# Optimization experiments

Measured on AMD Instinct MI355X. Metric: run time of the kernel, lower is better.

The kernel has to match this reference:

```python
import jax, jax.numpy as jnp
import numpy as np

V, E, NNZ = 50000, 25000, 200000
F_IN, HID, D = 128, 256, 4
H1, C = 16, 40  # h = [256, 16, 40] per the code's width schedule for l=2


def setup_inputs() -> dict:
    key = jax.random.key(0)
    ks = jax.random.split(key, 16)
    inp = {
        'x': jax.random.normal(ks[0], (V, F_IN), jnp.float32),
        'eattr': jax.random.normal(ks[1], (E, F_IN), jnp.float32),  # init_hedge='rand'
        'node_idx': jax.random.randint(ks[2], (NNZ,), 0, V),
        'edge_idx': jax.random.randint(ks[3], (NNZ,), 0, E),
        # lin: F_IN -> D*HID (shared for nodes and hyperedge attrs)
        'Wlin': jax.random.normal(ks[4], (F_IN, D * HID), jnp.float32) / np.sqrt(F_IN),
        'blin': jnp.zeros((D * HID,), jnp.float32),
        # diag sheaf builder: per-incidence, per-head restriction-map scalar
        'w1': jax.random.normal(ks[5], (HID, D), jnp.float32) / np.sqrt(HID),
        'w2': jax.random.normal(ks[6], (HID, D), jnp.float32) / np.sqrt(HID),
        'bs': jnp.zeros((D,), jnp.float32),
        # hypergraph conv layers
        'W0': jax.random.normal(ks[7], (HID, H1), jnp.float32) / np.sqrt(HID),
        'b0': jnp.zeros((H1,), jnp.float32),
        'W1': jax.random.normal(ks[8], (H1, C), jnp.float32) / np.sqrt(H1),
        'b1': jnp.zeros((C,), jnp.float32),
        # lin2: h[-1]*d -> num_classes, no bias
        'W2': jax.random.normal(ks[9], (D * C, C), jnp.float32) / np.sqrt(D * C),
    }
    return inp


def reference(x, eattr, node_idx, edge_idx, Wlin, blin, w1, w2, bs, W0, b0, W1, b1, W2):
    # lift node / hyperedge features into d stalks: [V, d, HID], [E, d, HID]
    Hn = (x @ Wlin + blin).reshape(V, D, HID)
    He = (eattr @ Wlin + blin).reshape(E, D, HID)

    # diagonal sheaf restriction maps, one scalar per (incidence, head)
    hv = Hn[node_idx]                      # [NNZ, D, HID] gather
    he = He[edge_idx]                      # [NNZ, D, HID] gather
    s = jnp.tanh(jnp.einsum('ndh,hd->nd', hv, w1)
                 + jnp.einsum('ndh,hd->nd', he, w2) + bs)   # [NNZ, D]

    # degree normalization (degree_norm): D^{-1}, inf -> 0
    deg_e = jax.ops.segment_sum(jnp.ones((NNZ,), jnp.float32), edge_idx, num_segments=E)
    inv_e = jnp.where(deg_e > 0, 1.0 / deg_e, 0.0)
    deg_v = jax.ops.segment_sum(jnp.ones((NNZ,), jnp.float32), node_idx, num_segments=V)
    inv_v = jnp.where(deg_v > 0, 1.0 / deg_v, 0.0)

    def apply_L(Hf):  # sheaf Laplacian L = I - D^{-1} F^T B F : [V, D, c] -> [V, D, c]
        m = jax.ops.segment_sum(s[:, :, None] * Hf[node_idx], edge_idx, num_segments=E)
        m = m * inv_e[:, None, None]       # hyperedge aggregation [E, D, c]
        a = jax.ops.segment_sum(s[:, :, None] * m[edge_idx], node_idx, num_segments=V)
        a = a * inv_v[:, None, None]       # back-scatter to nodes [V, D, c]
        return Hf - a

    H = jax.nn.relu(apply_L(Hn) @ W0 + b0)   # [V, D, 16]
    H = jax.nn.relu(apply_L(H) @ W1 + b1)    # [V, D, 40]
    return H.reshape(V, D * C) @ W2          # [V, 40]
```

## Files before the change

kernel.cpp:

```cpp
#include <hip/hip_runtime.h>
#include <hip/hip_fp16.h>
#include <stdint.h>

#define V_N 50000
#define E_N 25000
#define NNZ_N 200000
#define CHUNK 2048

__global__ __launch_bounds__(256) void k_zero(int* __restrict__ p, int n) {
  int i = blockIdx.x * 256 + threadIdx.x;
  if (i < n) p[i] = 0;
}

__global__ __launch_bounds__(64) void k_fuse(
    const float* __restrict__ Wlin, const float* __restrict__ blin,
    const float* __restrict__ w1, const float* __restrict__ w2,
    const float* __restrict__ bs, const float* __restrict__ W0,
    const float* __restrict__ b0,
    float* __restrict__ Wf0, float* __restrict__ u1, float* __restrict__ u2,
    float* __restrict__ cb, float* __restrict__ bf0, float* __restrict__ sbias)
{
  __shared__ float row[1024];
  __shared__ float W0s[4096];
  int f = blockIdx.x;
  for (int t = threadIdx.x; t < 1024; t += 64) row[t] = Wlin[f * 1024 + t];
  for (int t = threadIdx.x; t < 4096; t += 64) W0s[t] = W0[t];
  __syncthreads();
  int j = threadIdx.x;
  int d = j >> 4, jj = j & 15;
  float acc = 0.f;
  for (int h = 0; h < 256; ++h) acc += row[d * 256 + h] * W0s[h * 16 + jj];
  Wf0[f * 64 + j] = acc;
  if (j < 4) {
    float a1 = 0.f, a2 = 0.f;
    for (int h = 0; h < 256; ++h) {
      a1 += row[j * 256 + h] * w1[h * 4 + j];
      a2 += row[j * 256 + h] * w2[h * 4 + j];
    }
    u1[f * 4 + j] = a1;
    u2[f * 4 + j] = a2;
  }
  if (f == 0) {
    float ab = 0.f;
    for (int h = 0; h < 256; ++h) ab += blin[d * 256 + h] * W0s[h * 16 + jj];
    cb[j] = ab;
    bf0[j] = b0[jj];
    if (j < 4) {
      float sb = bs[j];
      for (int h = 0; h < 256; ++h) sb += blin[j * 256 + h] * (w1[h * 4 + j] + w2[h * 4 + j]);
      sbias[j] = sb;
    }
  }
}

__global__ __launch_bounds__(256) void k_degrees(
    const int* __restrict__ node_idx, const int* __restrict__ edge_idx,
    int* __restrict__ degE, int* __restrict__ degV)
{
  int i = blockIdx.x * 256 + threadIdx.x;
  if (i < NNZ_N) {
    atomicAdd(&degE[edge_idx[i]], 1);
    atomicAdd(&degV[node_idx[i]], 1);
  }
}

__global__ __launch_bounds__(256) void k_scanA(
    const int* __restrict__ degE, const int* __restrict__ degV,
    int* __restrict__ offE, int* __restrict__ offV,
    int* __restrict__ bsumE, int* __restrict__ bsumV, int nchunkE)
{
  bool isE = (int)blockIdx.x < nchunkE;
  const int* deg = isE ? degE : degV;
  int* off = isE ? offE : offV;
  int* bsum = isE ? bsumE : bsumV;
  int n = isE ? E_N : V_N;
  int chunk = isE ? blockIdx.x : (blockIdx.x - nchunkE);
  int base = chunk * CHUNK;
  int tid = threadIdx.x;
  int vals[8];
  int tsum = 0;
  for (int it = 0; it < 8; ++it) {
    int idx = base + tid * 8 + it;
    int v = (idx < n) ? deg[idx] : 0;
    vals[it] = tsum;
    tsum += v;
  }
  __shared__ int sA[256], sB[256];
  sA[tid] = tsum;
  __syncthreads();
  int* src = sA; int* dst = sB;
  for (int sh = 1; sh < 256; sh <<= 1) {
    dst[tid] = src[tid] + (tid >= sh ? src[tid - sh] : 0);
    __syncthreads();
    int* t = src; src = dst; dst = t;
  }
  int excl = src[tid] - tsum;
  for (int it = 0; it < 8; ++it) {
    int idx = base + tid * 8 + it;
    if (idx < n) off[idx] = excl + vals[it];
  }
  if (tid == 255) bsum[chunk] = src[255];
}

__global__ __launch_bounds__(64) void k_scanB(
    int* __restrict__ bsumE, int* __restrict__ bsumV, int nchunkE, int nchunkV)
{
  int* b = (blockIdx.x == 0) ? bsumE : bsumV;
  int n = (blockIdx.x == 0) ? nchunkE : nchunkV;
  int tid = threadIdx.x;
  int v = (tid < n) ? b[tid] : 0;
  int s = v;
  for (int sh = 1; sh < 64; sh <<= 1) {
    int o = __shfl_up(s, sh);
    if (tid >= sh) s += o;
  }
  if (tid < n) b[tid] = s - v;
}

__global__ __launch_bounds__(256) void k_scanC_inv(
    int* __restrict__ offE, int* __restrict__ offV,
    const int* __restrict__ bsumE, const int* __restrict__ bsumV,
    const int* __restrict__ degE, const int* __restrict__ degV,
    float* __restrict__ invE, float* __restrict__ invV, int nchunkE)
{
  bool isE = (int)blockIdx.x < nchunkE;
  int* off = isE ? offE : offV;
  const int* bsum = isE ? bsumE : bsumV;
  const int* deg = isE ? degE : degV;
  float* inv = isE ? invE : invV;
  int n = isE ? E_N : V_N;
  int chunk = isE ? blockIdx.x : (blockIdx.x - nchunkE);
  int base = chunk * CHUNK;
  int add = bsum[chunk];
  for (int it = 0; it < 8; ++it) {
    int idx = base + threadIdx.x * 8 + it;
    if (idx < n) {
      off[idx] += add;
      int dg = deg[idx];
      inv[idx] = dg > 0 ? 1.0f / (float)dg : 0.0f;
    }
  }
}

__global__ __launch_bounds__(256) void k_gemm_node(
    const float* __restrict__ x, const float* __restrict__ Wf0,
    const float* __restrict__ u1, const float* __restrict__ cb,
    __half* __restrict__ G0h, float* __restrict__ svx)
{
  __shared__ float Xt[64 * 132];
  __shared__ float us[512];
  int tid = threadIdx.x;
  int row0 = blockIdx.x * 64;
  #pragma unroll
  for (int it = 0; it < 8; ++it) {
    int fi = it * 1024 + tid * 4;
    int r = fi >> 7, c = fi & 127;
    float4 val = make_float4(0.f, 0.f, 0.f, 0.f);
    int gr = row0 + r;
    if (gr < V_N) val = *(const float4*)(x + (size_t)gr * 128 + c);
    *(float4*)&Xt[r * 132 + c] = val;
  }
  for (int k2 = tid; k2 < 512; k2 += 256) us[k2] = u1[k2];
  int ty = tid >> 4, tx = tid & 15;
  float4 cbr = *(const float4*)(cb + tx * 4);
  __syncthreads();

  float acc[4][4];
  #pragma unroll
  for (int i = 0; i < 4; ++i) {
    acc[i][0] = cbr.x; acc[i][1] = cbr.y; acc[i][2] = cbr.z; acc[i][3] = cbr.w;
  }
  #pragma unroll 2
  for (int k0 = 0; k0 < 128; k0 += 4) {
    float A_[4][4], W_[4][4];
    #pragma unroll
    for (int kk = 0; kk < 4; ++kk)
      *(float4*)&W_[kk][0] = *(const float4*)(Wf0 + (size_t)(k0 + kk) * 64 + tx * 4);
    #pragma unroll
    for (int i = 0; i < 4; ++i)
      *(float4*)&A_[i][0] = *(const float4*)&Xt[(ty * 4 + i) * 132 + k0];
    #pragma unroll
    for (int i = 0; i < 4; ++i)
      #pragma unroll
      for (int kk = 0; kk < 4; ++kk)
        #pragma unroll
        for (int j = 0; j < 4; ++j)
          acc[i][j] += A_[i][kk] * W_[kk][j];
  }
  #pragma unroll
  for (int i = 0; i < 4; ++i) {
    int gr = row0 + ty * 4 + i;
    if (gr < V_N) {
      __half2* dst = (__half2*)(G0h + (size_t)gr * 64 + tx * 4);
      dst[0] = __floats2half2_rn(acc[i][0], acc[i][1]);
      dst[1] = __floats2half2_rn(acc[i][2], acc[i][3]);
    }
  }
  int rs = tid >> 2, dS = tid & 3;
  float a2 = 0.f;
  for (int k = 0; k < 128; ++k)
    a2 += Xt[rs * 132 + k] * us[k * 4 + dS];
  int gr = row0 + rs;
  if (gr < V_N) svx[gr * 4 + dS] = a2;
}

__global__ __launch_bounds__(256) void k_gemm_edge(
    const float* __restrict__ eattr, const float* __restrict__ u2,
    float* __restrict__ sex)
{
  __shared__ float Xt[64 * 132];
  __shared__ float us[512];
  int tid = threadIdx.x;
  int row0 = blockIdx.x * 64;
  #pragma unroll
  for (int it = 0; it < 8; ++it) {
    int fi = it * 1024 + tid * 4;
    int r = fi >> 7, c = fi & 127;
    float4 val = make_float4(0.f, 0.f, 0.f, 0.f);
    int gr = row0 + r;
    if (gr < E_N) val = *(const float4*)(eattr + (size_t)gr * 128 + c);
    *(float4*)&Xt[r * 132 + c] = val;
  }
  for (int k2 = tid; k2 < 512; k2 += 256) us[k2] = u2[k2];
  __syncthreads();
  int rs = tid >> 2, dS = tid & 3;
  float a2 = 0.f;
  for (int k = 0; k < 128; ++k)
    a2 += Xt[rs * 132 + k] * us[k * 4 + dS];
  int gr = row0 + rs;
  if (gr < E_N) sex[gr * 4 + dS] = a2;
}

__global__ __launch_bounds__(256) void k_fill_s(
    const int* __restrict__ node_idx, const int* __restrict__ edge_idx,
    const int* __restrict__ offE, const int* __restrict__ offV,
    int* __restrict__ curE, int* __restrict__ curV,
    int* __restrict__ csrEv, int* __restrict__ csrVe,
    float* __restrict__ sE4, float* __restrict__ sV4,
    const float* __restrict__ svx, const float* __restrict__ sex,
    const float* __restrict__ sbias,
    const float* __restrict__ invE, const float* __restrict__ invV)
{
  int i = blockIdx.x * 256 + threadIdx.x;
  if (i >= NNZ_N) return;
  int v = node_idx[i], e = edge_idx[i];
  float4 a = *(const float4*)(svx + (size_t)v * 4);
  float4 b = *(const float4*)(sex + (size_t)e * 4);
  float4 sb = *(const float4*)(sbias);
  float4 r;
  r.x = tanhf(a.x + b.x + sb.x);
  r.y = tanhf(a.y + b.y + sb.y);
  r.z = tanhf(a.z + b.z + sb.z);
  r.w = tanhf(a.w + b.w + sb.w);
  float ie = invE[e], iv = invV[v];
  int pe = atomicAdd(&curE[e], 1);
  int slotE = offE[e] + pe;
  csrEv[slotE] = v;
  float4 re = make_float4(r.x * ie, r.y * ie, r.z * ie, r.w * ie);
  *(float4*)(sE4 + (size_t)slotE * 4) = re;
  int pv = atomicAdd(&curV[v], 1);
  int slotV = offV[v] + pv;
  csrVe[slotV] = e;
  float4 rv = make_float4(r.x * iv, r.y * iv, r.z * iv, r.w * iv);
  *(float4*)(sV4 + (size_t)slotV * 4) = rv;
}

__global__ __launch_bounds__(256) void k_eagg(
    const __half* __restrict__ Hin, const int* __restrict__ csrEv,
    const float* __restrict__ sE4,
    const int* __restrict__ offE, const int* __restrict__ degE,
    __half* __restrict__ m)
{
  int wave = threadIdx.x >> 6, lane = threadIdx.x & 63;
  int e = blockIdx.x * 4 + wave;
  if (e >= E_N) return;
  int o0 = offE[e], dg = degE[e];
  int hw = lane >> 3, L8 = lane & 7;
  int d = L8 >> 1;
  float4 a0 = make_float4(0.f, 0.f, 0.f, 0.f);
  float4 a1 = make_float4(0.f, 0.f, 0.f, 0.f);
  for (int base = 0; base < dg; base += 8) {
    int vv = 0;
    if (lane < 8 && base + lane < dg) vv = csrEv[o0 + base + lane];
    float ss = 0.f;
    if (lane < 32 && base * 4 + lane < dg * 4) ss = sE4[(size_t)o0 * 4 + base * 4 + lane];
    int tloc = base + hw;
    int v = __shfl(vv, hw);
    float sv = __shfl(ss, hw * 4 + d);
    if (tloc < dg) {
      uint4 raw = *(const uint4*)(Hin + (size_t)v * 64 + L8 * 8);
      float2 f0 = __half22float2(*reinterpret_cast<__half2*>(&raw.x));
      float2 f1 = __half22float2(*reinterpret_cast<__half2*>(&raw.y));
      float2 f2 = __half22float2(*reinterpret_cast<__half2*>(&raw.z));
      float2 f3 = __half22float2(*reinterpret_cast<__half2*>(&raw.w));
      a0.x += sv * f0.x; a0.y += sv * f0.y; a0.z += sv * f1.x; a0.w += sv * f1.y;
      a1.x += sv * f2.x; a1.y += sv * f2.y; a1.z += sv * f3.x; a1.w += sv * f3.y;
    }
  }
  #pragma unroll
  for (int off = 8; off <= 32; off <<= 1) {
    a0.x += __shfl_xor(a0.x, off); a0.y += __shfl_xor(a0.y, off);
    a0.z += __shfl_xor(a0.z, off); a0.w += __shfl_xor(a0.w, off);
    a1.x += __shfl_xor(a1.x, off); a1.y += __shfl_xor(a1.y, off);
    a1.z += __shfl_xor(a1.z, off); a1.w += __shfl_xor(a1.w, off);
  }
  if (hw == 0) {
    __half2 o0h = __floats2half2_rn(a0.x, a0.y);
    __half2 o1h = __floats2half2_rn(a0.z, a0.w);
    __half2 o2h = __floats2half2_rn(a1.x, a1.y);
    __half2 o3h = __floats2half2_rn(a1.z, a1.w);
    uint4 o;
    o.x = *(unsigned int*)&o0h; o.y = *(unsigned int*)&o1h;
    o.z = *(unsigned int*)&o2h; o.w = *(unsigned int*)&o3h;
    *(uint4*)(m + (size_t)e * 64 + L8 * 8) = o;
  }
}

__global__ __launch_bounds__(256) void k_nagg(
    const __half* __restrict__ base_, const __half* __restrict__ m,
    const int* __restrict__ csrVe, const float* __restrict__ sV4,
    const int* __restrict__ offV, const int* __restrict__ degV,
    const float* __restrict__ bf0, int doRelu,
    __half* __restrict__ outH, float* __restrict__ outF)
{
  int half = threadIdx.x >> 5;
  int v = blockIdx.x * 8 + half;
  if (v >= V_N) return;
  int lane = threadIdx.x & 63;
  int ll = lane & 31;
  int s0 = lane & 32;
  int o0 = offV[v], dg = degV[v];
  int hw = ll >> 3, L8 = ll & 7;
  int d = L8 >> 1;
  float4 a0 = make_float4(0.f, 0.f, 0.f, 0.f);
  float4 a1 = make_float4(0.f, 0.f, 0.f, 0.f);
  for (int base = 0; base < dg; base += 4) {
    int ee = 0;
    if (ll < 4 && base + ll < dg) ee = csrVe[o0 + base + ll];
    float ss = 0.f;
    if (ll < 16 && base * 4 + ll < dg * 4) ss = sV4[(size_t)o0 * 4 + base * 4 + ll];
    int tloc = base + hw;
    int e = __shfl(ee, s0 + hw);
    float sv = __shfl(ss, s0 + hw * 4 + d);
    if (tloc < dg) {
      uint4 raw = *(const uint4*)(m + (size_t)e * 64 + L8 * 8);
      float2 f0 = __half22float2(*reinterpret_cast<__half2*>(&raw.x));
      float2 f1 = __half22float2(*reinterpret_cast<__half2*>(&raw.y));
      float2 f2 = __half22float2(*reinterpret_cast<__half2*>(&raw.z));
      float2 f3 = __half22float2(*reinterpret_cast<__half2*>(&raw.w));
      a0.x += sv * f0.x; a0.y += sv * f0.y; a0.z += sv * f1.x; a0.w += sv * f1.y;
      a1.x += sv * f2.x; a1.y += sv * f2.y; a1.z += sv * f3.x; a1.w += sv * f3.y;
    }
  }
  #pragma unroll
  for (int off = 8; off <= 16; off <<= 1) {
    a0.x += __shfl_xor(a0.x, off); a0.y += __shfl_xor(a0.y, off);
    a0.z += __shfl_xor(a0.z, off); a0.w += __shfl_xor(a0.w, off);
    a1.x += __shfl_xor(a1.x, off); a1.y += __shfl_xor(a1.y, off);
    a1.z += __shfl_xor(a1.z, off); a1.w += __shfl_xor(a1.w, off);
  }
  if (hw == 0) {
    uint4 braw = *(const uint4*)(base_ + (size_t)v * 64 + L8 * 8);
    float2 b0f = __half22float2(*reinterpret_cast<__half2*>(&braw.x));
    float2 b1f = __half22float2(*reinterpret_cast<__half2*>(&braw.y));
    float2 b2f = __half22float2(*reinterpret_cast<__half2*>(&braw.z));
    float2 b3f = __half22float2(*reinterpret_cast<__half2*>(&braw.w));
    float r0 = b0f.x - a0.x, r1 = b0f.y - a0.y, r2 = b1f.x - a0.z, r3 = b1f.y - a0.w;
    float r4 = b2f.x - a1.x, r5 = b2f.y - a1.y, r6 = b3f.x - a1.z, r7 = b3f.y - a1.w;
    if (doRelu) {
      float4 bfa = *(const float4*)(bf0 + L8 * 8);
      float4 bfb = *(const float4*)(bf0 + L8 * 8 + 4);
      r0 = fmaxf(r0 + bfa.x, 0.f); r1 = fmaxf(r1 + bfa.y, 0.f);
      r2 = fmaxf(r2 + bfa.z, 0.f); r3 = fmaxf(r3 + bfa.w, 0.f);
      r4 = fmaxf(r4 + bfb.x, 0.f); r5 = fmaxf(r5 + bfb.y, 0.f);
      r6 = fmaxf(r6 + bfb.z, 0.f); r7 = fmaxf(r7 + bfb.w, 0.f);
      __half2 o0h = __floats2half2_rn(r0, r1);
      __half2 o1h = __floats2half2_rn(r2, r3);
      __half2 o2h = __floats2half2_rn(r4, r5);
      __half2 o3h = __floats2half2_rn(r6, r7);
      uint4 o;
      o.x = *(unsigned int*)&o0h; o.y = *(unsigned int*)&o1h;
      o.z = *(unsigned int*)&o2h; o.w = *(unsigned int*)&o3h;
      *(uint4*)(outH + (size_t)v * 64 + L8 * 8) = o;
    } else {
      *(float4*)(outF + (size_t)v * 64 + L8 * 8) = make_float4(r0, r1, r2, r3);
      *(float4*)(outF + (size_t)v * 64 + L8 * 8 + 4) = make_float4(r4, r5, r6, r7);
    }
  }
}

__global__ __launch_bounds__(256) void k_final(
    const float* __restrict__ A, const float* __restrict__ W1, const float* __restrict__ b1,
    const float* __restrict__ W2, float* __restrict__ out)
{
  __shared__ float W2s[160 * 40];
  __shared__ float t[32 * 164];
  __shared__ float W1s[640];
  __shared__ float b1s[40];
  int tid = threadIdx.x;
  int v0 = blockIdx.x * 32;

  for (int k = tid; k < 1600; k += 256) ((float4*)W2s)[k] = ((const float4*)W2)[k];
  for (int k = tid; k < 640; k += 256) W1s[k] = W1[k];
  if (tid < 40) b1s[tid] = b1[tid];
  __syncthreads();

  if (tid < 160) {
    int rg = tid / 20, cg = tid % 20;
    int r0 = rg * 4;
    int j0 = cg * 8;
    int d = cg / 5;
    int jloc = j0 - d * 40;
    float a[4][16];
    #pragma unroll
    for (int i = 0; i < 4; ++i) {
      int gr = v0 + r0 + i;
      #pragma unroll
      for (int c4 = 0; c4 < 4; ++c4) {
        float4 val = make_float4(0.f, 0.f, 0.f, 0.f);
        if (gr < V_N) val = *(const float4*)(A + (size_t)gr * 64 + d * 16 + c4 * 4);
        *(float4*)&a[i][c4 * 4] = val;
      }
    }
    float acc1[4][8];
    #pragma unroll
    for (int i = 0; i < 4; ++i)
      #pragma unroll
      for (int jj = 0; jj < 8; ++jj) acc1[i][jj] = b1s[jloc + jj];
    #pragma unroll
    for (int c = 0; c < 16; ++c) {
      float w[8];
      *(float4*)&w[0] = *(const float4*)&W1s[c * 40 + jloc];
      *(float4*)&w[4] = *(const float4*)&W1s[c * 40 + jloc + 4];
      #pragma unroll
      for (int i = 0; i < 4; ++i)
        #pragma unroll
        for (int jj = 0; jj < 8; ++jj)
          acc1[i][jj] += a[i][c] * w[jj];
    }
    #pragma unroll
    for (int i = 0; i < 4; ++i) {
      float4 lo = make_float4(fmaxf(acc1[i][0], 0.f), fmaxf(acc1[i][1], 0.f),
                              fmaxf(acc1[i][2], 0.f), fmaxf(acc1[i][3], 0.f));
      float4 hi = make_float4(fmaxf(acc1[i][4], 0.f), fmaxf(acc1[i][5], 0.f),
                              fmaxf(acc1[i][6], 0.f), fmaxf(acc1[i][7], 0.f));
      *(float4*)&t[(r0 + i) * 164 + j0] = lo;
      *(float4*)&t[(r0 + i) * 164 + j0 + 4] = hi;
    }
  }
  __syncthreads();

  if (tid < 160) {
    int rg2 = tid / 10, cg2 = tid % 10;
    float acc2[2][4] = {{0.f, 0.f, 0.f, 0.f}, {0.f, 0.f, 0.f, 0.f}};
    for (int k0 = 0; k0 < 160; k0 += 4) {
      float a0[4], a1[4], w[4][4];
      *(float4*)a0 = *(const float4*)&t[(rg2 * 2 + 0) * 164 + k0];
      *(float4*)a1 = *(const float4*)&t[(rg2 * 2 + 1) * 164 + k0];
      #pragma unroll
      for (int kk = 0; kk < 4; ++kk)
        *(float4*)&w[kk][0] = *(const float4*)&W2s[(k0 + kk) * 40 + cg2 * 4];
      #pragma unroll
      for (int kk = 0; kk < 4; ++kk)
        #pragma unroll
        for (int j = 0; j < 4; ++j) {
          acc2[0][j] += a0[kk] * w[kk][j];
          acc2[1][j] += a1[kk] * w[kk][j];
        }
    }
    #pragma unroll
    for (int i = 0; i < 2; ++i) {
      int gr = v0 + rg2 * 2 + i;
      if (gr < V_N)
        *(float4*)(out + (size_t)gr * 40 + cg2 * 4) =
            make_float4(acc2[i][0], acc2[i][1], acc2[i][2], acc2[i][3]);
    }
  }
}

extern "C" void kernel_launch(void* const* d_in, const int* in_sizes, int n_in,
                              void* d_out, int out_size, void* d_ws, size_t ws_size,
                              hipStream_t stream) {
  (void)in_sizes; (void)n_in; (void)out_size; (void)ws_size;
  const float* x = (const float*)d_in[0];
  const float* eattr = (const float*)d_in[1];
  const int* node_idx = (const int*)d_in[2];
  const int* edge_idx = (const int*)d_in[3];
  const float* Wlin = (const float*)d_in[4];
  const float* blin = (const float*)d_in[5];
  const float* w1 = (const float*)d_in[6];
  const float* w2 = (const float*)d_in[7];
  const float* bs = (const float*)d_in[8];
  const float* W0 = (const float*)d_in[9];
  const float* b0 = (const float*)d_in[10];
  const float* W1 = (const float*)d_in[11];
  const float* b1 = (const float*)d_in[12];
  const float* W2 = (const float*)d_in[13];
  float* out = (float*)d_out;

  char* p = (char*)d_ws;
  auto alloc = [&](size_t bytes) { char* q = p; p += (bytes + 255) & ~(size_t)255; return q; };
  float*  Wf0   = (float*)alloc(8192 * 4);
  float*  u1    = (float*)alloc(512 * 4);
  float*  u2    = (float*)alloc(512 * 4);
  float*  cbv   = (float*)alloc(64 * 4);
  float*  bf0   = (float*)alloc(64 * 4);
  float*  sbias = (float*)alloc(4 * 4);
  __half* G0h   = (__half*)alloc((size_t)V_N * 64 * 2);
  __half* Hbh   = (__half*)alloc((size_t)V_N * 64 * 2);
  __half* mbh   = (__half*)alloc((size_t)E_N * 64 * 2);
  float*  Af    = (float*)alloc((size_t)V_N * 64 * 4);
  float*  svx   = (float*)alloc((size_t)V_N * 4 * 4);
  float*  sex   = (float*)alloc((size_t)E_N * 4 * 4);
  float*  sE4   = (float*)alloc((size_t)NNZ_N * 4 * 4);
  float*  sV4   = (float*)alloc((size_t)NNZ_N * 4 * 4);
  float*  invE  = (float*)alloc(E_N * 4);
  float*  invV  = (float*)alloc(V_N * 4);
  int* zeroRegion = (int*)alloc((size_t)(2 * E_N + 2 * V_N) * 4);
  int* degE = zeroRegion;
  int* degV = degE + E_N;
  int* curE = degV + V_N;
  int* curV = curE + E_N;
  int* offE  = (int*)alloc(E_N * 4);
  int* offV  = (int*)alloc(V_N * 4);
  int* csrEv = (int*)alloc((size_t)NNZ_N * 4);
  int* csrVe = (int*)alloc((size_t)NNZ_N * 4);
  int* bsumE = (int*)alloc(64 * 4);
  int* bsumV = (int*)alloc(64 * 4);

  int nZero = 2 * E_N + 2 * V_N;
  int nchunkE = (E_N + CHUNK - 1) / CHUNK;
  int nchunkV = (V_N + CHUNK - 1) / CHUNK;
  int nbNode = (V_N + 63) / 64;
  int nbEdge = (E_N + 63) / 64;

  hipLaunchKernelGGL(k_zero, dim3((nZero + 255) / 256), dim3(256), 0, stream, zeroRegion, nZero);
  hipLaunchKernelGGL(k_fuse, dim3(128), dim3(64), 0, stream,
                     Wlin, blin, w1, w2, bs, W0, b0, Wf0, u1, u2, cbv, bf0, sbias);
  hipLaunchKernelGGL(k_degrees, dim3((NNZ_N + 255) / 256), dim3(256), 0, stream,
                     node_idx, edge_idx, degE, degV);
  hipLaunchKernelGGL(k_scanA, dim3(nchunkE + nchunkV), dim3(256), 0, stream,
                     degE, degV, offE, offV, bsumE, bsumV, nchunkE);
  hipLaunchKernelGGL(k_scanB, dim3(2), dim3(64), 0, stream, bsumE, bsumV, nchunkE, nchunkV);
  hipLaunchKernelGGL(k_scanC_inv, dim3(nchunkE + nchunkV), dim3(256), 0, stream,
                     offE, offV, bsumE, bsumV, degE, degV, invE, invV, nchunkE);
  hipLaunchKernelGGL(k_gemm_node, dim3(nbNode), dim3(256), 0, stream,
                     x, Wf0, u1, cbv, G0h, svx);
  hipLaunchKernelGGL(k_gemm_edge, dim3(nbEdge), dim3(256), 0, stream,
                     eattr, u2, sex);
  hipLaunchKernelGGL(k_fill_s, dim3((NNZ_N + 255) / 256), dim3(256), 0, stream,
                     node_idx, edge_idx, offE, offV, curE, curV, csrEv, csrVe,
                     sE4, sV4, svx, sex, sbias, invE, invV);
  hipLaunchKernelGGL(k_eagg, dim3((E_N + 3) / 4), dim3(256), 0, stream,
                     G0h, csrEv, sE4, offE, degE, mbh);
  hipLaunchKernelGGL(k_nagg, dim3((V_N + 7) / 8), dim3(256), 0, stream,
                     G0h, mbh, csrVe, sV4, offV, degV, bf0, 1, Hbh, (float*)nullptr);
  hipLaunchKernelGGL(k_eagg, dim3((E_N + 3) / 4), dim3(256), 0, stream,
                     Hbh, csrEv, sE4, offE, degE, mbh);
  hipLaunchKernelGGL(k_nagg, dim3((V_N + 7) / 8), dim3(256), 0, stream,
                     Hbh, mbh, csrVe, sV4, offV, degV, bf0, 0, (__half*)nullptr, Af);
  hipLaunchKernelGGL(k_final, dim3((V_N + 31) / 32), dim3(256), 0, stream, Af, W1, b1, W2, out);
}
```

Baseline: 284.1 us.

## Merge CSR build and aggregation kernels into one cooperative persistent kernel

Replaces the zero, degree, three scan, fill, and four aggregation launches with a single cooperative kernel of 768 blocks that uses grid-wide syncs between phases. The goal is to remove per-launch overhead and the idle gaps between many small dependent kernels. In exchange, every phase now runs on a fixed persistent grid with grid-stride loops, and each grid.sync adds a barrier cost. Occupancy is capped by the launch_bounds(256,3) hint, which can limit latency hiding in the gather-heavy aggregation phases.

New measurement: 1.047 ms. 268% more time.

```diff
diff --git a/kernel.cpp b/kernel.cpp
--- a/kernel.cpp
+++ b/kernel.cpp
@@ -1,16 +1,14 @@
 #include <hip/hip_runtime.h>
 #include <hip/hip_fp16.h>
+#include <hip/hip_cooperative_groups.h>
 #include <stdint.h>
+
+namespace cg = cooperative_groups;
 
 #define V_N 50000
 #define E_N 25000
 #define NNZ_N 200000
 #define CHUNK 2048
-
-__global__ __launch_bounds__(256) void k_zero(int* __restrict__ p, int n) {
-  int i = blockIdx.x * 256 + threadIdx.x;
-  if (i < n) p[i] = 0;
-}
 
 __global__ __launch_bounds__(64) void k_fuse(
     const float* __restrict__ Wlin, const float* __restrict__ blin,
@@ -53,95 +51,6 @@
   }
 }
 
-__global__ __launch_bounds__(256) void k_degrees(
-    const int* __restrict__ node_idx, const int* __restrict__ edge_idx,
-    int* __restrict__ degE, int* __restrict__ degV)
-{
-  int i = blockIdx.x * 256 + threadIdx.x;
-  if (i < NNZ_N) {
-    atomicAdd(&degE[edge_idx[i]], 1);
-    atomicAdd(&degV[node_idx[i]], 1);
-  }
-}
-
-__global__ __launch_bounds__(256) void k_scanA(
-    const int* __restrict__ degE, const int* __restrict__ degV,
-    int* __restrict__ offE, int* __restrict__ offV,
-    int* __restrict__ bsumE, int* __restrict__ bsumV, int nchunkE)
-{
-  bool isE = (int)blockIdx.x < nchunkE;
-  const int* deg = isE ? degE : degV;
-  int* off = isE ? offE : offV;
-  int* bsum = isE ? bsumE : bsumV;
-  int n = isE ? E_N : V_N;
-  int chunk = isE ? blockIdx.x : (blockIdx.x - nchunkE);
-  int base = chunk * CHUNK;
-  int tid = threadIdx.x;
-  int vals[8];
-  int tsum = 0;
-  for (int it = 0; it < 8; ++it) {
-    int idx = base + tid * 8 + it;
-    int v = (idx < n) ? deg[idx] : 0;
-    vals[it] = tsum;
-    tsum += v;
-  }
-  __shared__ int sA[256], sB[256];
-  sA[tid] = tsum;
-  __syncthreads();
-  int* src = sA; int* dst = sB;
-  for (int sh = 1; sh < 256; sh <<= 1) {
-    dst[tid] = src[tid] + (tid >= sh ? src[tid - sh] : 0);
-    __syncthreads();
-    int* t = src; src = dst; dst = t;
-  }
-  int excl = src[tid] - tsum;
-  for (int it = 0; it < 8; ++it) {
-    int idx = base + tid * 8 + it;
-    if (idx < n) off[idx] = excl + vals[it];
-  }
-  if (tid == 255) bsum[chunk] = src[255];
-}
-
-__global__ __launch_bounds__(64) void k_scanB(
-    int* __restrict__ bsumE, int* __restrict__ bsumV, int nchunkE, int nchunkV)
-{
-  int* b = (blockIdx.x == 0) ? bsumE : bsumV;
-  int n = (blockIdx.x == 0) ? nchunkE : nchunkV;
-  int tid = threadIdx.x;
-  int v = (tid < n) ? b[tid] : 0;
-  int s = v;
-  for (int sh = 1; sh < 64; sh <<= 1) {
-    int o = __shfl_up(s, sh);
-    if (tid >= sh) s += o;
-  }
-  if (tid < n) b[tid] = s - v;
-}
-
-__global__ __launch_bounds__(256) void k_scanC_inv(
-    int* __restrict__ offE, int* __restrict__ offV,
-    const int* __restrict__ bsumE, const int* __restrict__ bsumV,
-    const int* __restrict__ degE, const int* __restrict__ degV,
-    float* __restrict__ invE, float* __restrict__ invV, int nchunkE)
-{
-  bool isE = (int)blockIdx.x < nchunkE;
-  int* off = isE ? offE : offV;
-  const int* bsum = isE ? bsumE : bsumV;
-  const int* deg = isE ? degE : degV;
-  float* inv = isE ? invE : invV;
-  int n = isE ? E_N : V_N;
-  int chunk = isE ? blockIdx.x : (blockIdx.x - nchunkE);
-  int base = chunk * CHUNK;
-  int add = bsum[chunk];
-  for (int it = 0; it < 8; ++it) {
-    int idx = base + threadIdx.x * 8 + it;
-    if (idx < n) {
-      off[idx] += add;
-      int dg = deg[idx];
-      inv[idx] = dg > 0 ? 1.0f / (float)dg : 0.0f;
-    }
-  }
-}
-
 __global__ __launch_bounds__(256) void k_gemm_node(
     const float* __restrict__ x, const float* __restrict__ Wf0,
     const float* __restrict__ u1, const float* __restrict__ cb,
@@ -231,49 +140,11 @@
   if (gr < E_N) sex[gr * 4 + dS] = a2;
 }
 
-__global__ __launch_bounds__(256) void k_fill_s(
-    const int* __restrict__ node_idx, const int* __restrict__ edge_idx,
-    const int* __restrict__ offE, const int* __restrict__ offV,
-    int* __restrict__ curE, int* __restrict__ curV,
-    int* __restrict__ csrEv, int* __restrict__ csrVe,
-    float* __restrict__ sE4, float* __restrict__ sV4,
-    const float* __restrict__ svx, const float* __restrict__ sex,
-    const float* __restrict__ sbias,
-    const float* __restrict__ invE, const float* __restrict__ invV)
-{
-  int i = blockIdx.x * 256 + threadIdx.x;
-  if (i >= NNZ_N) return;
-  int v = node_idx[i], e = edge_idx[i];
-  float4 a = *(const float4*)(svx + (size_t)v * 4);
-  float4 b = *(const float4*)(sex + (size_t)e * 4);
-  float4 sb = *(const float4*)(sbias);
-  float4 r;
-  r.x = tanhf(a.x + b.x + sb.x);
-  r.y = tanhf(a.y + b.y + sb.y);
-  r.z = tanhf(a.z + b.z + sb.z);
-  r.w = tanhf(a.w + b.w + sb.w);
-  float ie = invE[e], iv = invV[v];
-  int pe = atomicAdd(&curE[e], 1);
-  int slotE = offE[e] + pe;
-  csrEv[slotE] = v;
-  float4 re = make_float4(r.x * ie, r.y * ie, r.z * ie, r.w * ie);
-  *(float4*)(sE4 + (size_t)slotE * 4) = re;
-  int pv = atomicAdd(&curV[v], 1);
-  int slotV = offV[v] + pv;
-  csrVe[slotV] = e;
-  float4 rv = make_float4(r.x * iv, r.y * iv, r.z * iv, r.w * iv);
-  *(float4*)(sV4 + (size_t)slotV * 4) = rv;
-}
-
-__global__ __launch_bounds__(256) void k_eagg(
-    const __half* __restrict__ Hin, const int* __restrict__ csrEv,
-    const float* __restrict__ sE4,
-    const int* __restrict__ offE, const int* __restrict__ degE,
-    __half* __restrict__ m)
-{
-  int wave = threadIdx.x >> 6, lane = threadIdx.x & 63;
-  int e = blockIdx.x * 4 + wave;
-  if (e >= E_N) return;
+__device__ __forceinline__ void eagg_seg(
+    int e, const __half* __restrict__ Hin, const int* __restrict__ csrEv,
+    const float* __restrict__ sE4, const int* __restrict__ offE,
+    const int* __restrict__ degE, __half* __restrict__ m, int lane)
+{
   int o0 = offE[e], dg = degE[e];
   int hw = lane >> 3, L8 = lane & 7;
   int d = L8 >> 1;
@@ -316,17 +187,13 @@
   }
 }
 
-__global__ __launch_bounds__(256) void k_nagg(
-    const __half* __restrict__ base_, const __half* __restrict__ m,
+__device__ __forceinline__ void nagg_seg(
+    int v, const __half* __restrict__ base_, const __half* __restrict__ m,
     const int* __restrict__ csrVe, const float* __restrict__ sV4,
     const int* __restrict__ offV, const int* __restrict__ degV,
-    const float* __restrict__ bf0, int doRelu,
-    __half* __restrict__ outH, float* __restrict__ outF)
-{
-  int half = threadIdx.x >> 5;
-  int v = blockIdx.x * 8 + half;
-  if (v >= V_N) return;
-  int lane = threadIdx.x & 63;
+    const float* __restrict__ bf0, bool doRelu,
+    __half* __restrict__ outH, float* __restrict__ outF, int lane)
+{
   int ll = lane & 31;
   int s0 = lane & 32;
   int o0 = offV[v], dg = degV[v];
@@ -389,6 +256,153 @@
   }
 }
 
+__global__ __launch_bounds__(256, 3) void k_mega(
+    const int* __restrict__ node_idx, const int* __restrict__ edge_idx,
+    const float* __restrict__ svx, const float* __restrict__ sex,
+    const float* __restrict__ sbias, const float* __restrict__ bf0,
+    int* __restrict__ zeroReg,
+    int* __restrict__ offE, int* __restrict__ offV,
+    int* __restrict__ bsumE, int* __restrict__ bsumV,
+    float* __restrict__ invE, float* __restrict__ invV,
+    int* __restrict__ csrEv, int* __restrict__ csrVe,
+    float* __restrict__ sE4, float* __restrict__ sV4,
+    const __half* __restrict__ G0h, __half* __restrict__ Hbh,
+    __half* __restrict__ mbh, float* __restrict__ Af)
+{
+  cg::grid_group grid = cg::this_grid();
+  int tid = threadIdx.x;
+  const int NB = gridDim.x;
+  const int NT = NB * 256;
+  int gid = blockIdx.x * 256 + tid;
+
+  int* degE = zeroReg;
+  int* degV = degE + E_N;
+  int* curE = degV + V_N;
+  int* curV = curE + E_N;
+
+  __shared__ int sA[256], sB[256];
+
+  for (int i = gid; i < 2 * E_N + 2 * V_N; i += NT) zeroReg[i] = 0;
+  grid.sync();
+
+  for (int i = gid; i < NNZ_N; i += NT) {
+    atomicAdd(&degE[edge_idx[i]], 1);
+    atomicAdd(&degV[node_idx[i]], 1);
+  }
+  grid.sync();
+
+  const int nchE = (E_N + CHUNK - 1) / CHUNK;
+  const int nchV = (V_N + CHUNK - 1) / CHUNK;
+  for (int blk = blockIdx.x; blk < nchE + nchV; blk += NB) {
+    bool isE = blk < nchE;
+    const int* deg = isE ? degE : degV;
+    int* off = isE ? offE : offV;
+    int* bsum = isE ? bsumE : bsumV;
+    int n = isE ? E_N : V_N;
+    int chunk = isE ? blk : blk - nchE;
+    int base = chunk * CHUNK;
+    int vals[8];
+    int tsum = 0;
+    for (int it = 0; it < 8; ++it) {
+      int idx = base + tid * 8 + it;
+      int v = (idx < n) ? deg[idx] : 0;
+      vals[it] = tsum;
+      tsum += v;
+    }
+    __syncthreads();
+    sA[tid] = tsum;
+    __syncthreads();
+    int* src = sA; int* dst = sB;
+    for (int sh = 1; sh < 256; sh <<= 1) {
+      dst[tid] = src[tid] + (tid >= sh ? src[tid - sh] : 0);
+      __syncthreads();
+      int* t = src; src = dst; dst = t;
+    }
+    int excl = src[tid] - tsum;
+    for (int it = 0; it < 8; ++it) {
+      int idx = base + tid * 8 + it;
+      if (idx < n) off[idx] = excl + vals[it];
+    }
+    if (tid == 255) bsum[chunk] = src[255];
+  }
+  grid.sync();
+
+  if (blockIdx.x < 2 && tid < 64) {
+    int* b = (blockIdx.x == 0) ? bsumE : bsumV;
+    int n = (blockIdx.x == 0) ? nchE : nchV;
+    int v = (tid < n) ? b[tid] : 0;
+    int s = v;
+    for (int sh = 1; sh < 64; sh <<= 1) {
+      int o = __shfl_up(s, sh);
+      if (tid >= sh) s += o;
+    }
+    if (tid < n) b[tid] = s - v;
+  }
+  grid.sync();
+
+  for (int blk = blockIdx.x; blk < nchE + nchV; blk += NB) {
+    bool isE = blk < nchE;
+    int* off = isE ? offE : offV;
+    const int* bsum = isE ? bsumE : bsumV;
+    const int* deg = isE ? degE : degV;
+    float* inv = isE ? invE : invV;
+    int n = isE ? E_N : V_N;
+    int chunk = isE ? blk : blk - nchE;
+    int base = chunk * CHUNK;
+    int add = bsum[chunk];
+    for (int it = 0; it < 8; ++it) {
+      int idx = base + tid * 8 + it;
+      if (idx < n) {
+        off[idx] += add;
+        int dg = deg[idx];
+        inv[idx] = dg > 0 ? 1.0f / (float)dg : 0.0f;
+      }
+    }
+  }
+  grid.sync();
+
+  for (int i = gid; i < NNZ_N; i += NT) {
+    int v = node_idx[i], e = edge_idx[i];
+    float4 a = *(const float4*)(svx + (size_t)v * 4);
+    float4 b = *(const float4*)(sex + (size_t)e * 4);
+    float4 sb = *(const float4*)(sbias);
+    float4 r;
+    r.x = tanhf(a.x + b.x + sb.x);
+    r.y = tanhf(a.y + b.y + sb.y);
+    r.z = tanhf(a.z + b.z + sb.z);
+    r.w = tanhf(a.w + b.w + sb.w);
+    float ie = invE[e], iv = invV[v];
+    int pe = atomicAdd(&curE[e], 1);
+    int slotE = offE[e] + pe;
+    csrEv[slotE] = v;
+    *(float4*)(sE4 + (size_t)slotE * 4) = make_float4(r.x * ie, r.y * ie, r.z * ie, r.w * ie);
+    int pv = atomicAdd(&curV[v], 1);
+    int slotV = offV[v] + pv;
+    csrVe[slotV] = e;
+    *(float4*)(sV4 + (size_t)slotV * 4) = make_float4(r.x * iv, r.y * iv, r.z * iv, r.w * iv);
+  }
+  grid.sync();
+
+  int lane = tid & 63;
+  int waveG = blockIdx.x * 4 + (tid >> 6);
+  int halfG = blockIdx.x * 8 + (tid >> 5);
+
+  for (int e = waveG; e < E_N; e += NB * 4)
+    eagg_seg(e, G0h, csrEv, sE4, offE, degE, mbh, lane);
+  grid.sync();
+
+  for (int v = halfG; v < V_N; v += NB * 8)
+    nagg_seg(v, G0h, mbh, csrVe, sV4, offV, degV, bf0, true, Hbh, (float*)nullptr, lane);
+  grid.sync();
+
+  for (int e = waveG; e < E_N; e += NB * 4)
+    eagg_seg(e, Hbh, csrEv, sE4, offE, degE, mbh, lane);
+  grid.sync();
+
+  for (int v = halfG; v < V_N; v += NB * 8)
+    nagg_seg(v, Hbh, mbh, csrVe, sV4, offV, degV, bf0, false, (__half*)nullptr, Af, lane);
+}
+
 __global__ __launch_bounds__(256) void k_final(
     const float* __restrict__ A, const float* __restrict__ W1, const float* __restrict__ b1,
     const float* __restrict__ W2, float* __restrict__ out)
@@ -406,10 +420,10 @@
   __syncthreads();
 
   if (tid < 160) {
-    int rg = tid / 20, cg = tid % 20;
+    int rg = tid / 20, cg2 = tid % 20;
     int r0 = rg * 4;
-    int j0 = cg * 8;
-    int d = cg / 5;
+    int j0 = cg2 * 8;
+    int d = cg2 / 5;
     int jloc = j0 - d * 40;
     float a[4][16];
     #pragma unroll
@@ -517,10 +531,6 @@
   float*  invE  = (float*)alloc(E_N * 4);
   float*  invV  = (float*)alloc(V_N * 4);
   int* zeroRegion = (int*)alloc((size_t)(2 * E_N + 2 * V_N) * 4);
-  int* degE = zeroRegion;
-  int* degV = degE + E_N;
-  int* curE = degV + V_N;
-  int* curV = curE + E_N;
   int* offE  = (int*)alloc(E_N * 4);
   int* offV  = (int*)alloc(V_N * 4);
   int* csrEv = (int*)alloc((size_t)NNZ_N * 4);
@@ -528,36 +538,25 @@
   int* bsumE = (int*)alloc(64 * 4);
   int* bsumV = (int*)alloc(64 * 4);
 
-  int nZero = 2 * E_N + 2 * V_N;
-  int nchunkE = (E_N + CHUNK - 1) / CHUNK;
-  int nchunkV = (V_N + CHUNK - 1) / CHUNK;
   int nbNode = (V_N + 63) / 64;
   int nbEdge = (E_N + 63) / 64;
 
-  hipLaunchKernelGGL(k_zero, dim3((nZero + 255) / 256), dim3(256), 0, stream, zeroRegion, nZero);
   hipLaunchKernelGGL(k_fuse, dim3(128), dim3(64), 0, stream,
                      Wlin, blin, w1, w2, bs, W0, b0, Wf0, u1, u2, cbv, bf0, sbias);
-  hipLaunchKernelGGL(k_degrees, dim3((NNZ_N + 255) / 256), dim3(256), 0, stream,
-                     node_idx, edge_idx, degE, degV);
-  hipLaunchKernelGGL(k_scanA, dim3(nchunkE + nchunkV), dim3(256), 0, stream,
-                     degE, degV, offE, offV, bsumE, bsumV, nchunkE);
-  hipLaunchKernelGGL(k_scanB, dim3(2), dim3(64), 0, stream, bsumE, bsumV, nchunkE, nchunkV);
-  hipLaunchKernelGGL(k_scanC_inv, dim3(nchunkE + nchunkV), dim3(256), 0, stream,
-                     offE, offV, bsumE, bsumV, degE, degV, invE, invV, nchunkE);
   hipLaunchKernelGGL(k_gemm_node, dim3(nbNode), dim3(256), 0, stream,
                      x, Wf0, u1, cbv, G0h, svx);
   hipLaunchKernelGGL(k_gemm_edge, dim3(nbEdge), dim3(256), 0, stream,
                      eattr, u2, sex);
-  hipLaunchKernelGGL(k_fill_s, dim3((NNZ_N + 255) / 256), dim3(256), 0, stream,
-                     node_idx, edge_idx, offE, offV, curE, curV, csrEv, csrVe,
-                     sE4, sV4, svx, sex, sbias, invE, invV);
-  hipLaunchKernelGGL(k_eagg, dim3((E_N + 3) / 4), dim3(256), 0, stream,
-                     G0h, csrEv, sE4, offE, degE, mbh);
-  hipLaunchKernelGGL(k_nagg, dim3((V_N + 7) / 8), dim3(256), 0, stream,
-                     G0h, mbh, csrVe, sV4, offV, degV, bf0, 1, Hbh, (float*)nullptr);
-  hipLaunchKernelGGL(k_eagg, dim3((E_N + 3) / 4), dim3(256), 0, stream,
-                     Hbh, csrEv, sE4, offE, degE, mbh);
-  hipLaunchKernelGGL(k_nagg, dim3((V_N + 7) / 8), dim3(256), 0, stream,
-                     Hbh, mbh, csrVe, sV4, offV, degV, bf0, 0, (__half*)nullptr, Af);
+
+  void* args[] = {
+    (void*)&node_idx, (void*)&edge_idx, (void*)&svx, (void*)&sex,
+    (void*)&sbias, (void*)&bf0, (void*)&zeroRegion,
+    (void*)&offE, (void*)&offV, (void*)&bsumE, (void*)&bsumV,
+    (void*)&invE, (void*)&invV, (void*)&csrEv, (void*)&csrVe,
+    (void*)&sE4, (void*)&sV4, (void*)&G0h, (void*)&Hbh,
+    (void*)&mbh, (void*)&Af
+  };
+  hipLaunchCooperativeKernel((const void*)k_mega, dim3(768), dim3(256), args, 0, stream);
+
   hipLaunchKernelGGL(k_final, dim3((V_N + 31) / 32), dim3(256), 0, stream, Af, W1, b1, W2, out);
 }
```
